# Kernel optimization log

Measured on AMD Instinct MI355X. Metric: run time of the kernel, lower is better.

## Reference

```python
import jax, jax.numpy as jnp
import numpy as np

B, L, D = 2, 2048, 2048        # batch, seqlen, d_model
DIN, N, R, K = 4096, 16, 128, 4  # d_inner, d_state, dt_rank, d_conv


def setup_inputs() -> dict:
    key = jax.random.key(0)
    ks = jax.random.split(key, 9)
    hidden_states = jax.random.normal(ks[0], (B, L, D), dtype=jnp.float32) * 0.02
    in_proj_w = jax.random.normal(ks[1], (2 * DIN, D), dtype=jnp.float32) * (1.0 / np.sqrt(D))
    conv1d_w = jax.random.normal(ks[2], (DIN, K), dtype=jnp.float32) * (1.0 / np.sqrt(DIN))
    x_proj_w = jax.random.normal(ks[3], (R + 2 * N, DIN), dtype=jnp.float32) * (1.0 / np.sqrt(DIN))
    dt_proj_w = jax.random.normal(ks[4], (DIN, R), dtype=jnp.float32) * (1.0 / np.sqrt(R))
    # dt_proj_bias init: inverse-softplus of dt ~ LogUniform(1e-3, 1e-1), as in init_dtprojbias
    dt = jnp.exp(jax.random.uniform(ks[5], (DIN,)) * (np.log(0.1) - np.log(0.001)) + np.log(0.001))
    dt = jnp.clip(dt, 1e-4, None)
    dt_proj_bias = dt + jnp.log(-jnp.expm1(-dt))
    # A_log init: log(arange(1..N)) broadcast over d_inner (init_A)
    A_log = jnp.broadcast_to(jnp.log(jnp.arange(1, N + 1, dtype=jnp.float32)), (DIN, N))
    D_param = jnp.ones((DIN,), dtype=jnp.float32)
    out_proj_w = jax.random.normal(ks[6], (D, DIN), dtype=jnp.float32) * (1.0 / np.sqrt(DIN))
    return {
        "hidden_states": hidden_states, "in_proj_w": in_proj_w, "conv1d_w": conv1d_w,
        "x_proj_w": x_proj_w, "dt_proj_w": dt_proj_w, "dt_proj_bias": dt_proj_bias,
        "A_log": A_log, "D_param": D_param, "out_proj_w": out_proj_w,
    }


def _mamba_forward(hidden_states, in_proj_w, conv1d_w, x_proj_w, dt_proj_w,
                   dt_proj_bias, A_log, D_param, out_proj_w):
    b, l, _ = hidden_states.shape
    # in_proj: (b,l,d_model) -> (b,l,2*d_inner), split into x and gate z
    xz = jnp.einsum("bld,ed->ble", hidden_states, in_proj_w)
    x, z = jnp.split(xz, 2, axis=-1)  # each (b,l,d_inner)

    # depthwise causal conv1d along l, no bias, then SiLU
    xp = jnp.pad(x, ((0, 0), (K - 1, 0), (0, 0)))
    xc = sum(conv1d_w[:, k] * xp[:, k:k + l, :] for k in range(K))  # (b,l,d_inner)
    xc = jax.nn.silu(xc)

    # x_proj -> dt_rank + 2*d_state, split into dt, B, C
    x_dbl = jnp.einsum("bld,ed->ble", xc, x_proj_w)
    dt_r = x_dbl[..., :R]                    # (b,l,R)
    Bc = x_dbl[..., R:R + N]                 # (b,l,N)
    Cc = x_dbl[..., R + N:]                  # (b,l,N)
    delta = jax.nn.softplus(jnp.einsum("blr,dr->bld", dt_r, dt_proj_w) + dt_proj_bias)  # (b,l,d_inner)

    A = -jnp.exp(A_log)  # (d_inner, N)

    # selective scan: h_t = exp(delta_t*A)*h_{t-1} + delta_t*x_t*B_t; y_t = <h_t, C_t>
    def step(h, inp):
        delta_t, B_t, C_t, x_t = inp  # (b,d), (b,n), (b,n), (b,d)
        dA = jnp.exp(delta_t[..., None] * A)                 # (b,d,n)
        h = h * dA + (delta_t * x_t)[..., None] * B_t[:, None, :]
        y_t = jnp.einsum("bdn,bn->bd", h, C_t)
        return h, y_t

    inputs = (jnp.swapaxes(delta, 0, 1), jnp.swapaxes(Bc, 0, 1),
              jnp.swapaxes(Cc, 0, 1), jnp.swapaxes(xc, 0, 1))
    h0 = jnp.zeros((b, DIN, N), dtype=xc.dtype)
    _, y = jax.lax.scan(step, h0, inputs)     # y: (l,b,d_inner)
    y = jnp.swapaxes(y, 0, 1)                 # (b,l,d_inner)

    y = y + xc * D_param                      # skip term
    y = y * jax.nn.silu(z)                    # gating
    return jnp.einsum("bld,ed->ble", y, out_proj_w)  # (b,l,d_model)


def reference(hidden_states, in_proj_w, conv1d_w, x_proj_w, dt_proj_w,
              dt_proj_bias, A_log, D_param, out_proj_w):
    return _mamba_forward(hidden_states, in_proj_w, conv1d_w, x_proj_w, dt_proj_w,
                          dt_proj_bias, A_log, D_param, out_proj_w)
```

## Files before the change

### kernel.cpp

```cpp
#include <hip/hip_runtime.h>
#include <math.h>

#define DIN   4096
#define NST   16
#define RR    128
#define LSEQ  2048
#define NTOK  4096
#define BB    2
#define CHUNK 64
#define NCH   (LSEQ / CHUNK)
#define KSPL  8
#define KC    (DIN / KSPL)

typedef __attribute__((ext_vector_type(8))) short short8;
typedef __attribute__((ext_vector_type(4))) float f32x4;

__device__ __forceinline__ float sigmoidf_(float x) { return 1.f / (1.f + __expf(-x)); }
__device__ __forceinline__ float softplusf_(float x) {
    return fmaxf(x, 0.f) + log1pf(__expf(-fabsf(x)));
}
__device__ __forceinline__ unsigned short f2bf_(float f) {
    unsigned u = __float_as_uint(f);
    return (unsigned short)((u + 0x7FFFu + ((u >> 16) & 1u)) >> 16);
}
__device__ __forceinline__ void gld_lds16_(const unsigned short* g, unsigned short* l) {
    __builtin_amdgcn_global_load_lds((const __attribute__((address_space(1))) unsigned int*)g,
                                     (__attribute__((address_space(3))) unsigned int*)l,
                                     16, 0, 0);
}

__global__ __launch_bounds__(256)
void f2bf_kernel(const float* __restrict__ src, unsigned short* __restrict__ dst, int n8)
{
    int i = blockIdx.x * 256 + threadIdx.x;
    if (i >= n8) return;
    const float4* s = (const float4*)src + 2 * (size_t)i;
    float4 a = s[0], b = s[1];
    union { unsigned short u[8]; uint4 v; } o;
    o.u[0] = f2bf_(a.x); o.u[1] = f2bf_(a.y); o.u[2] = f2bf_(a.z); o.u[3] = f2bf_(a.w);
    o.u[4] = f2bf_(b.x); o.u[5] = f2bf_(b.y); o.u[6] = f2bf_(b.z); o.u[7] = f2bf_(b.w);
    ((uint4*)dst)[i] = o.v;
}


#define BAR()        asm volatile("s_barrier" ::: "memory")
#define WAIT_LGKM0() asm volatile("s_waitcnt lgkmcnt(0)" ::: "memory")
#define WAIT_VM(n)   asm volatile("s_waitcnt vmcnt(" #n ")" ::: "memory")


#define RD_A(P, mh) do { _Pragma("unroll") \
  for (int ii = 0; ii < 4; ++ii) { \
      aF[ii][0] = *(const short8*)((P) + (mh)*8192 + ii*2048 + co0); \
      aF[ii][1] = *(const short8*)((P) + (mh)*8192 + ii*2048 + co1); } } while (0)

#define RD_B(P, nh, DST) do { _Pragma("unroll") \
  for (int jj = 0; jj < 2; ++jj) { \
      DST[jj][0] = *(const short8*)((P) + (nh)*4096 + jj*2048 + co0); \
      DST[jj][1] = *(const short8*)((P) + (nh)*4096 + jj*2048 + co1); } } while (0)

#define MFMA_Q(mh, nh, BF) do { __builtin_amdgcn_s_setprio(1); _Pragma("unroll") \
  for (int ii = 0; ii < 4; ++ii) { _Pragma("unroll") \
    for (int jj = 0; jj < 2; ++jj) { _Pragma("unroll") \
      for (int ks = 0; ks < 2; ++ks) \
        acc[(mh)*4+ii][(nh)*2+jj] = __builtin_amdgcn_mfma_f32_16x16x32_bf16( \
            aF[ii][ks], BF[jj][ks], acc[(mh)*4+ii][(nh)*2+jj], 0, 0, 0); } } \
  __builtin_amdgcn_s_setprio(0); } while (0)

#define STGLD(gbase, sbase, h, l, tile) \
  gld_lds16_(gbase + (size_t)((h)*128 + (l)*64) * K + (size_t)(tile)*64, \
             (unsigned short*)(sbase + (h)*16384 + (l)*8192))

#define ITER(t, PREF) do { \
   \
  RD_A(pA0, 0); RD_B(pB0c, 0, bA); \
  STGLD(gA0, sA1, 1, 0, (t)+1); STGLD(gA0, sA1, 1, 1, (t)+1); \
  BAR(); WAIT_LGKM0(); MFMA_Q(0, 0, bA); BAR(); \
   \
  RD_B(pB0c, 1, bB); \
  BAR(); WAIT_LGKM0(); MFMA_Q(0, 1, bB); BAR(); \
   \
  RD_A(pA0, 1); \
  if (PREF) { STGLD(gB0, sB0, 0, 0, (t)+2); STGLD(gB0, sB0, 0, 1, (t)+2); } \
  BAR(); WAIT_LGKM0(); MFMA_Q(1, 1, bB); BAR(); \
   \
  if (PREF) { STGLD(gA0, sA0, 0, 0, (t)+2); STGLD(gA0, sA0, 0, 1, (t)+2); \
              STGLD(gB0, sB0, 1, 0, (t)+2); STGLD(gB0, sB0, 1, 1, (t)+2); } \
  BAR(); WAIT_LGKM0(); MFMA_Q(1, 0, bA); \
  if (PREF) { WAIT_VM(6); } else { WAIT_VM(0); } \
  BAR(); \
   \
  RD_A(pA1, 0); RD_B(pB1c, 0, bA); \
  if (PREF) { STGLD(gA0, sA0, 1, 0, (t)+2); STGLD(gA0, sA0, 1, 1, (t)+2); } \
  BAR(); WAIT_LGKM0(); MFMA_Q(0, 0, bA); BAR(); \
   \
  RD_B(pB1c, 1, bB); \
  BAR(); WAIT_LGKM0(); MFMA_Q(0, 1, bB); BAR(); \
   \
  RD_A(pA1, 1); \
  if (PREF) { STGLD(gB0, sB1, 0, 0, (t)+3); STGLD(gB0, sB1, 0, 1, (t)+3); } \
  BAR(); WAIT_LGKM0(); MFMA_Q(1, 1, bB); BAR(); \
   \
  if (PREF) { STGLD(gA0, sA1, 0, 0, (t)+3); STGLD(gA0, sA1, 0, 1, (t)+3); \
              STGLD(gB0, sB1, 1, 0, (t)+3); STGLD(gB0, sB1, 1, 1, (t)+3); } \
  BAR(); WAIT_LGKM0(); MFMA_Q(1, 0, bA); \
  if (PREF) { WAIT_VM(6); } else { WAIT_VM(0); } \
  BAR(); \
} while (0)

template<int MODE>
__global__ __launch_bounds__(512)
void gemm256(const unsigned short* __restrict__ A, const unsigned short* __restrict__ W,
             float* __restrict__ C, int K, int ldc, float* __restrict__ C2,
             int nbx, int fx)
{
    __shared__ __align__(16) unsigned short sm[65536];
    char* smb = (char*)sm;

    const int tid = threadIdx.x;
    const int ln  = tid & 63;
    const int wv  = tid >> 6;
    const int wm  = wv >> 2;
    const int wn  = wv & 3;
    const int m15 = ln & 15;
    const int q   = ln >> 4;

    const int bid = blockIdx.x;
    const int xcd = bid & 7;
    const int idx = bid >> 3;
    const int cw  = nbx / fx;
    const int chh = (gridDim.x >> 3) / cw;
    const int bn_i = (xcd % fx) * cw  + idx % cw;
    const int bm_i = (xcd / fx) * chh + idx / cw;
    const int bm  = bm_i << 8;
    const int bn  = bn_i << 8;

    const int co0 = (q * 16) ^ ((m15 & 7) << 4);
    const int co1 = co0 ^ 64;
    const int ra_base = wm * 16384 + m15 * 128;
    const int rb_base = wn * 8192  + m15 * 128;
    const char* pA0  = smb + ra_base;
    const char* pA1  = smb + 65536 + ra_base;
    const char* pB0c = smb + 32768 + rb_base;
    const char* pB1c = smb + 98304 + rb_base;

    char* sA0 = smb +          tid * 16;
    char* sB0 = smb + 32768  + tid * 16;
    char* sA1 = smb + 65536  + tid * 16;
    char* sB1 = smb + 98304  + tid * 16;
    const int srow  = tid >> 3;
    const int secol = (((tid & 7) ^ ((tid >> 3) & 7)) * 8);
    const unsigned short* gA0 = A + (size_t)(bm + srow) * K + secol;
    const unsigned short* gB0 = W + (size_t)(bn + srow) * K + secol;

    f32x4  acc[8][4] = {};
    short8 aF[4][2], bA[2][2], bB[2][2];

    const int KT = K >> 6;

    STGLD(gA0, sA0, 0, 0, 0); STGLD(gA0, sA0, 0, 1, 0);
    STGLD(gA0, sA0, 1, 0, 0); STGLD(gA0, sA0, 1, 1, 0);
    STGLD(gB0, sB0, 0, 0, 0); STGLD(gB0, sB0, 0, 1, 0);
    STGLD(gB0, sB0, 1, 0, 0); STGLD(gB0, sB0, 1, 1, 0);
    STGLD(gA0, sA1, 0, 0, 1); STGLD(gA0, sA1, 0, 1, 1);
    STGLD(gB0, sB1, 0, 0, 1); STGLD(gB0, sB1, 0, 1, 1);
    STGLD(gB0, sB1, 1, 0, 1); STGLD(gB0, sB1, 1, 1, 1);
    WAIT_VM(6);
    BAR();

    for (int t = 0; t < KT - 2; t += 2) ITER(t, 1);
    ITER(KT - 2, 0);

    float* Cp = C;
    int bcol = bn;
    if (MODE == 2 && bcol >= DIN) { Cp = C2; bcol -= DIN; }
    #pragma unroll
    for (int i = 0; i < 8; ++i) {
        int row = bm + wm * 128 + i * 16 + q * 4;
        #pragma unroll
        for (int j = 0; j < 4; ++j) {
            int col = bcol + wn * 64 + j * 16 + m15;
            #pragma unroll
            for (int r = 0; r < 4; ++r)
                Cp[(size_t)(row + r) * ldc + col] = acc[i][j][r];
        }
    }
}

template<int MODE>
__global__ __launch_bounds__(256)
void gemm_mfma_bt(const unsigned short* __restrict__ A, const unsigned short* __restrict__ W,
                  float* __restrict__ C, int K, int ldc,
                  const float* __restrict__ bias, float* __restrict__ C2)
{
    __shared__ unsigned short As[128 * 32];
    __shared__ unsigned short Ws[128 * 32];
    const int tid = threadIdx.x;
    const int bm = blockIdx.y << 7;
    int bn = blockIdx.x << 7;

    const int c0 = tid, c1 = tid + 256;
    const unsigned short* ga0 = A + (size_t)(bm + (c0 >> 2)) * K + (c0 & 3) * 8;
    const unsigned short* ga1 = A + (size_t)(bm + (c1 >> 2)) * K + (c1 & 3) * 8;
    const unsigned short* gw0 = W + (size_t)(bn + (c0 >> 2)) * K + (c0 & 3) * 8;
    const unsigned short* gw1 = W + (size_t)(bn + (c1 >> 2)) * K + (c1 & 3) * 8;
    unsigned short* la0 = &As[c0 * 8];
    unsigned short* la1 = &As[c1 * 8];
    unsigned short* lw0 = &Ws[c0 * 8];
    unsigned short* lw1 = &Ws[c1 * 8];

    const int ln  = tid & 63;
    const int wv  = tid >> 6;
    const int wm  = (wv >> 1) << 6;
    const int wn  = (wv & 1) << 6;
    const int m15 = ln & 15;
    const int q   = ln >> 4;

    f32x4 acc[4][4] = {};

    for (int k0 = 0; k0 < K; k0 += 32) {
        __syncthreads();
        gld_lds16_(ga0, la0); gld_lds16_(ga1, la1);
        gld_lds16_(gw0, lw0); gld_lds16_(gw1, lw1);
        ga0 += 32; ga1 += 32; gw0 += 32; gw1 += 32;
        __syncthreads();
        short8 af[4], wf[4];
        #pragma unroll
        for (int i = 0; i < 4; ++i)
            af[i] = *(const short8*)&As[(wm + i * 16 + m15) * 32 + q * 8];
        #pragma unroll
        for (int j = 0; j < 4; ++j)
            wf[j] = *(const short8*)&Ws[(wn + j * 16 + m15) * 32 + q * 8];
        #pragma unroll
        for (int i = 0; i < 4; ++i)
            #pragma unroll
            for (int j = 0; j < 4; ++j)
                acc[i][j] = __builtin_amdgcn_mfma_f32_16x16x32_bf16(af[i], wf[j],
                                                                    acc[i][j], 0, 0, 0);
    }

    float* Cp = C;
    if (MODE == 2 && bn >= DIN) { Cp = C2; bn -= DIN; }

    #pragma unroll
    for (int i = 0; i < 4; ++i)
        #pragma unroll
        for (int j = 0; j < 4; ++j) {
            int col = bn + wn + j * 16 + m15;
            #pragma unroll
            for (int r = 0; r < 4; ++r) {
                int row = bm + wm + i * 16 + q * 4 + r;
                float v = acc[i][j][r];
                if (MODE == 1) v = softplusf_(v + bias[col]);
                Cp[(size_t)row * ldc + col] = v;
            }
        }
}

__global__ __launch_bounds__(256)
void gemm_kspl_kernel(const float* __restrict__ A, const float* __restrict__ W,
                      float* __restrict__ partial)
{
    __shared__ float As[16][66];
    __shared__ float Ws[16][162];
    const int tid = threadIdx.x;
    const int tx = tid & 15;
    const int ty = tid >> 4;
    const int bm = blockIdx.x << 6;
    const int k0 = blockIdx.y * KC;

    float acc[4][10] = {};

    for (int kt = 0; kt < KC; kt += 16) {
        float2 a2[2];
        #pragma unroll
        for (int i = 0; i < 2; ++i) {
            int idx = tid + 256 * i;
            int row = idx >> 3, kofs = (idx & 7) * 2;
            a2[i] = *(const float2*)&A[(size_t)(bm + row) * DIN + k0 + kt + kofs];
        }
        float2 w2[5];
        #pragma unroll
        for (int i = 0; i < 5; ++i) {
            int idx = tid + 256 * i;
            int wrow = idx >> 3, wk = (idx & 7) * 2;
            w2[i] = *(const float2*)&W[(size_t)wrow * DIN + k0 + kt + wk];
        }
        __syncthreads();
        #pragma unroll
        for (int i = 0; i < 2; ++i) {
            int idx = tid + 256 * i;
            int row = idx >> 3, kofs = (idx & 7) * 2;
            As[kofs][row] = a2[i].x; As[kofs + 1][row] = a2[i].y;
        }
        #pragma unroll
        for (int i = 0; i < 5; ++i) {
            int idx = tid + 256 * i;
            int wrow = idx >> 3, wk = (idx & 7) * 2;
            Ws[wk][wrow] = w2[i].x; Ws[wk + 1][wrow] = w2[i].y;
        }
        __syncthreads();
        #pragma unroll
        for (int kk = 0; kk < 16; ++kk) {
            float2 av0 = *(const float2*)&As[kk][ty * 4];
            float2 av1 = *(const float2*)&As[kk][ty * 4 + 2];
            float a[4] = {av0.x, av0.y, av1.x, av1.y};
            float w[10];
            #pragma unroll
            for (int j = 0; j < 5; ++j) {
                float2 wv = *(const float2*)&Ws[kk][tx * 10 + 2 * j];
                w[2 * j] = wv.x; w[2 * j + 1] = wv.y;
            }
            #pragma unroll
            for (int i = 0; i < 4; ++i)
                #pragma unroll
                for (int j = 0; j < 10; ++j)
                    acc[i][j] = fmaf(a[i], w[j], acc[i][j]);
        }
        __syncthreads();
    }

    float* po = partial + (size_t)blockIdx.y * NTOK * 160;
    #pragma unroll
    for (int i = 0; i < 4; ++i) {
        int r = bm + ty * 4 + i;
        #pragma unroll
        for (int j = 0; j < 5; ++j)
            *(float2*)&po[(size_t)r * 160 + tx * 10 + 2 * j] =
                make_float2(acc[i][2 * j], acc[i][2 * j + 1]);
    }
}

__global__ __launch_bounds__(256)
void kspl_reduce_kernel(const float* __restrict__ partial, float* __restrict__ xdbl,
                        unsigned short* __restrict__ dtr)
{
    int idx = blockIdx.x * 256 + threadIdx.x;
    float s = 0.f;
    #pragma unroll
    for (int k = 0; k < KSPL; ++k)
        s += partial[(size_t)k * NTOK * 160 + idx];
    xdbl[idx] = s;
    int row = idx / 160;
    int col = idx - row * 160;
    if (col < RR) dtr[(size_t)row * RR + col] = f2bf_(s);
}

__global__ __launch_bounds__(256)
void conv_silu_kernel(const float* __restrict__ x, const float* __restrict__ cw,
                      float* __restrict__ xc)
{
    int idx = blockIdx.x * 256 + threadIdx.x;
    int d = idx & (DIN - 1);
    int tok = idx >> 12;
    int t = tok & (LSEQ - 1);
    float w0 = cw[d * 4 + 0], w1 = cw[d * 4 + 1];
    float w2 = cw[d * 4 + 2], w3 = cw[d * 4 + 3];
    const float* xp = x + (size_t)tok * DIN + d;
    float acc = w3 * xp[0];
    if (t >= 1) acc = fmaf(w2, xp[-DIN], acc);
    if (t >= 2) acc = fmaf(w1, xp[-2 * DIN], acc);
    if (t >= 3) acc = fmaf(w0, xp[-3 * DIN], acc);
    xc[idx] = acc * sigmoidf_(acc);
}

__global__ __launch_bounds__(256)
void scan_part1_kernel(const float* __restrict__ delta, const float* __restrict__ xc,
                       const float* __restrict__ xdbl, const float* __restrict__ A_log,
                       float* __restrict__ hloc, float* __restrict__ ssum)
{
    int d = blockIdx.x * 256 + threadIdx.x;
    int c = blockIdx.y;
    int b = blockIdx.z;
    float A[NST], h[NST];
    #pragma unroll
    for (int n = 0; n < NST; ++n) {
        A[n] = -__expf(A_log[d * NST + n]);
        h[n] = 0.f;
    }
    float s = 0.f;
    int tok = b * LSEQ + c * CHUNK;
    for (int t = 0; t < CHUNK; ++t, ++tok) {
        float dv = delta[(size_t)tok * DIN + d];
        float xv = xc[(size_t)tok * DIN + d];
        const float* bc = xdbl + (size_t)tok * 160 + RR;
        float dx = dv * xv;
        s += dv;
        #pragma unroll
        for (int n = 0; n < NST; ++n)
            h[n] = fmaf(h[n], __expf(dv * A[n]), dx * bc[n]);
    }
    size_t base = (size_t)(b * NCH + c) * NST * DIN + d;
    #pragma unroll
    for (int n = 0; n < NST; ++n) hloc[base + (size_t)n * DIN] = h[n];
    ssum[(size_t)(b * NCH + c) * DIN + d] = s;
}

__global__ __launch_bounds__(256)
void scan_part2_kernel(float* __restrict__ hloc, const float* __restrict__ ssum,
                       const float* __restrict__ A_log)
{
    int idx = blockIdx.x * 256 + threadIdx.x;
    int b = idx >> 12;
    int d = idx & (DIN - 1);
    float A[NST], hin[NST];
    #pragma unroll
    for (int n = 0; n < NST; ++n) {
        A[n] = -__expf(A_log[d * NST + n]);
        hin[n] = 0.f;
    }
    for (int c = 0; c < NCH; ++c) {
        size_t base = (size_t)(b * NCH + c) * NST * DIN + d;
        float s = ssum[(size_t)(b * NCH + c) * DIN + d];
        #pragma unroll
        for (int n = 0; n < NST; ++n) {
            float hl = hloc[base + (size_t)n * DIN];
            hloc[base + (size_t)n * DIN] = hin[n];
            hin[n] = fmaf(hin[n], __expf(A[n] * s), hl);
        }
    }
}

__global__ __launch_bounds__(256)
void scan_part3_kernel(const float* __restrict__ delta, float* __restrict__ xcy,
                       const float* __restrict__ xdbl, const float* __restrict__ z,
                       const float* __restrict__ A_log, const float* __restrict__ Dp,
                       const float* __restrict__ hin_buf)
{
    int d = blockIdx.x * 256 + threadIdx.x;
    int c = blockIdx.y;
    int b = blockIdx.z;
    float A[NST], h[NST];
    size_t base = (size_t)(b * NCH + c) * NST * DIN + d;
    #pragma unroll
    for (int n = 0; n < NST; ++n) {
        A[n] = -__expf(A_log[d * NST + n]);
        h[n] = hin_buf[base + (size_t)n * DIN];
    }
    float Dv = Dp[d];
    int tok = b * LSEQ + c * CHUNK;
    for (int t = 0; t < CHUNK; ++t, ++tok) {
        float dv = delta[(size_t)tok * DIN + d];
        float xv = xcy[(size_t)tok * DIN + d];
        float zv = z[(size_t)tok * DIN + d];
        const float* bc = xdbl + (size_t)tok * 160 + RR;
        float dx = dv * xv;
        float y = 0.f;
        #pragma unroll
        for (int n = 0; n < NST; ++n) {
            h[n] = fmaf(h[n], __expf(dv * A[n]), dx * bc[n]);
            y = fmaf(h[n], bc[NST + n], y);
        }
        y = (y + xv * Dv) * (zv * sigmoidf_(zv));
        xcy[(size_t)tok * DIN + d] = y;
    }
}

extern "C" void kernel_launch(void* const* d_in, const int* in_sizes, int n_in,
                              void* d_out, int out_size, void* d_ws, size_t ws_size,
                              hipStream_t stream)
{
    const float* hidden     = (const float*)d_in[0];
    const float* in_proj_w  = (const float*)d_in[1];
    const float* conv_w     = (const float*)d_in[2];
    const float* x_proj_w   = (const float*)d_in[3];
    const float* dt_proj_w  = (const float*)d_in[4];
    const float* dt_bias    = (const float*)d_in[5];
    const float* A_log      = (const float*)d_in[6];
    const float* D_param    = (const float*)d_in[7];
    const float* out_proj_w = (const float*)d_in[8];
    float* out = (float*)d_out;

    const size_t BIG = (size_t)NTOK * DIN * sizeof(float);
    char* ws = (char*)d_ws;
    float* xbuf = (float*)(ws);
    float* xc   = (float*)(ws + BIG);
    float* zbuf = (float*)(ws + 2 * BIG);
    float* xdbl = (float*)(ws + 3 * BIG);
    float* delta = xbuf;

    unsigned short* w_in_bf  = (unsigned short*)xc;
    unsigned short* hid_bf   = (unsigned short*)out;
    unsigned short* y_bf     = (unsigned short*)xbuf;
    unsigned short* w_out_bf = (unsigned short*)zbuf;

    float* xpart = out;
    unsigned short* dtr_bf = (unsigned short*)(out + (size_t)KSPL * NTOK * 160);
    unsigned short* dtw_bf = dtr_bf + (size_t)NTOK * RR;
    float* hloc  = out;
    float* ssum  = out + (size_t)BB * NCH * NST * DIN;

    f2bf_kernel<<<8192, 256, 0, stream>>>(in_proj_w, w_in_bf, (2 * DIN * 2048) / 8);
    f2bf_kernel<<<4096, 256, 0, stream>>>(hidden, hid_bf, (NTOK * 2048) / 8);
    gemm256<2><<<512, 512, 0, stream>>>(hid_bf, w_in_bf, xbuf, 2048, DIN, zbuf, 32, 4);
    conv_silu_kernel<<<(NTOK * DIN) / 256, 256, 0, stream>>>(xbuf, conv_w, xc);
    gemm_kspl_kernel<<<dim3(NTOK / 64, KSPL), 256, 0, stream>>>(xc, x_proj_w, xpart);
    kspl_reduce_kernel<<<(NTOK * 160) / 256, 256, 0, stream>>>(xpart, xdbl, dtr_bf);
    f2bf_kernel<<<256, 256, 0, stream>>>(dt_proj_w, dtw_bf, (DIN * RR) / 8);
    gemm_mfma_bt<1><<<dim3(32, 32), 256, 0, stream>>>(dtr_bf, dtw_bf, delta,
                                                      RR, DIN, dt_bias, nullptr);
    scan_part1_kernel<<<dim3(DIN / 256, NCH, BB), 256, 0, stream>>>(delta, xc, xdbl,
                                                                    A_log, hloc, ssum);
    scan_part2_kernel<<<(BB * DIN) / 256, 256, 0, stream>>>(hloc, ssum, A_log);
    scan_part3_kernel<<<dim3(DIN / 256, NCH, BB), 256, 0, stream>>>(delta, xc, xdbl,
                                                                    zbuf, A_log, D_param, hloc);
    f2bf_kernel<<<8192, 256, 0, stream>>>(xc, y_bf, (NTOK * DIN) / 8);
    f2bf_kernel<<<4096, 256, 0, stream>>>(out_proj_w, w_out_bf, (2048 * DIN) / 8);
    gemm256<0><<<128, 512, 0, stream>>>(y_bf, w_out_bf, out, 4096, 2048, nullptr, 8, 2);
}
```

Baseline: 744.4 us.

## Split-K the out_proj GEMM and prefetch LDS fragments across MFMA phases

The out_proj GEMM previously launched only 128 blocks on a 256-CU-class GPU. It now splits K into two halves (MODE 3, 256 blocks), writes the second half's partial into a scratch buffer (xc), and sums the halves with a new float4 add kernel. Separately, the GEMM main loop is reordered so LDS fragment reads for the next quarter are issued right after the current MFMA group, with the first reads hoisted before the loop. This overlaps LDS latency with matrix math and removes some barrier stalls. The cost is an extra 32MB read-modify-write pass and more code in the barrier schedule.

```diff
diff --git a/kernel.cpp b/kernel.cpp
--- a/kernel.cpp
+++ b/kernel.cpp
@@ -42,6 +42,17 @@
     ((uint4*)dst)[i] = o.v;
 }
 
+__global__ __launch_bounds__(256)
+void add_f4_kernel(float* __restrict__ dst, const float* __restrict__ src, int n4)
+{
+    int i = blockIdx.x * 256 + threadIdx.x;
+    if (i >= n4) return;
+    float4 a = ((const float4*)dst)[i];
+    float4 b = ((const float4*)src)[i];
+    a.x += b.x; a.y += b.y; a.z += b.z; a.w += b.w;
+    ((float4*)dst)[i] = a;
+}
+
 
 #define BAR()        asm volatile("s_barrier" ::: "memory")
 #define WAIT_LGKM0() asm volatile("s_waitcnt lgkmcnt(0)" ::: "memory")
@@ -72,45 +83,51 @@
 
 #define ITER(t, PREF) do { \
    \
-  RD_A(pA0, 0); RD_B(pB0c, 0, bA); \
   STGLD(gA0, sA1, 1, 0, (t)+1); STGLD(gA0, sA1, 1, 1, (t)+1); \
-  BAR(); WAIT_LGKM0(); MFMA_Q(0, 0, bA); BAR(); \
-   \
-  RD_B(pB0c, 1, bB); \
-  BAR(); WAIT_LGKM0(); MFMA_Q(0, 1, bB); BAR(); \
-   \
-  RD_A(pA0, 1); \
+  BAR(); WAIT_LGKM0(); MFMA_Q(0, 0, bA); \
+  RD_B(pB0c, 1, bB);                     \
+  BAR(); \
+   \
+  BAR(); WAIT_LGKM0(); MFMA_Q(0, 1, bB); \
+  RD_A(pA0, 1);                          \
+  BAR(); \
+   \
   if (PREF) { STGLD(gB0, sB0, 0, 0, (t)+2); STGLD(gB0, sB0, 0, 1, (t)+2); } \
-  BAR(); WAIT_LGKM0(); MFMA_Q(1, 1, bB); BAR(); \
+  BAR(); WAIT_LGKM0(); MFMA_Q(1, 1, bB); \
+  BAR(); \
    \
   if (PREF) { STGLD(gA0, sA0, 0, 0, (t)+2); STGLD(gA0, sA0, 0, 1, (t)+2); \
               STGLD(gB0, sB0, 1, 0, (t)+2); STGLD(gB0, sB0, 1, 1, (t)+2); } \
   BAR(); WAIT_LGKM0(); MFMA_Q(1, 0, bA); \
   if (PREF) { WAIT_VM(6); } else { WAIT_VM(0); } \
-  BAR(); \
-   \
-  RD_A(pA1, 0); RD_B(pB1c, 0, bA); \
+  RD_A(pA1, 0); RD_B(pB1c, 0, bA);       \
+  BAR(); \
+   \
   if (PREF) { STGLD(gA0, sA0, 1, 0, (t)+2); STGLD(gA0, sA0, 1, 1, (t)+2); } \
-  BAR(); WAIT_LGKM0(); MFMA_Q(0, 0, bA); BAR(); \
-   \
-  RD_B(pB1c, 1, bB); \
-  BAR(); WAIT_LGKM0(); MFMA_Q(0, 1, bB); BAR(); \
-   \
-  RD_A(pA1, 1); \
+  BAR(); WAIT_LGKM0(); MFMA_Q(0, 0, bA); \
+  RD_B(pB1c, 1, bB);                     \
+  BAR(); \
+   \
+  BAR(); WAIT_LGKM0(); MFMA_Q(0, 1, bB); \
+  RD_A(pA1, 1);                          \
+  BAR(); \
+   \
   if (PREF) { STGLD(gB0, sB1, 0, 0, (t)+3); STGLD(gB0, sB1, 0, 1, (t)+3); } \
-  BAR(); WAIT_LGKM0(); MFMA_Q(1, 1, bB); BAR(); \
+  BAR(); WAIT_LGKM0(); MFMA_Q(1, 1, bB); \
+  BAR(); \
    \
   if (PREF) { STGLD(gA0, sA1, 0, 0, (t)+3); STGLD(gA0, sA1, 0, 1, (t)+3); \
               STGLD(gB0, sB1, 1, 0, (t)+3); STGLD(gB0, sB1, 1, 1, (t)+3); } \
   BAR(); WAIT_LGKM0(); MFMA_Q(1, 0, bA); \
   if (PREF) { WAIT_VM(6); } else { WAIT_VM(0); } \
+  if (PREF) { RD_A(pA0, 0); RD_B(pB0c, 0, bA); } \
   BAR(); \
 } while (0)
 
 template<int MODE>
 __global__ __launch_bounds__(512)
 void gemm256(const unsigned short* __restrict__ A, const unsigned short* __restrict__ W,
-             float* __restrict__ C, int K, int ldc, float* __restrict__ C2,
+             float* __restrict__ C, int K, int KL, int ldc, float* __restrict__ C2,
              int nbx, int fx)
 {
     __shared__ __align__(16) unsigned short sm[65536];
@@ -130,7 +147,9 @@
     const int cw  = nbx / fx;
     const int chh = (gridDim.x >> 3) / cw;
     const int bn_i = (xcd % fx) * cw  + idx % cw;
-    const int bm_i = (xcd / fx) * chh + idx / cw;
+    int bm_i = (xcd / fx) * chh + idx / cw;
+    int kh = 0;
+    if (MODE == 3) { kh = bm_i >> 4; bm_i &= 15; }
     const int bm  = bm_i << 8;
     const int bn  = bn_i << 8;
 
@@ -149,13 +168,13 @@
     char* sB1 = smb + 98304  + tid * 16;
     const int srow  = tid >> 3;
     const int secol = (((tid & 7) ^ ((tid >> 3) & 7)) * 8);
-    const unsigned short* gA0 = A + (size_t)(bm + srow) * K + secol;
-    const unsigned short* gB0 = W + (size_t)(bn + srow) * K + secol;
+    const unsigned short* gA0 = A + (size_t)(bm + srow) * K + secol + (size_t)kh * KL;
+    const unsigned short* gB0 = W + (size_t)(bn + srow) * K + secol + (size_t)kh * KL;
 
     f32x4  acc[8][4] = {};
     short8 aF[4][2], bA[2][2], bB[2][2];
 
-    const int KT = K >> 6;
+    const int KT = KL >> 6;
 
     STGLD(gA0, sA0, 0, 0, 0); STGLD(gA0, sA0, 0, 1, 0);
     STGLD(gA0, sA0, 1, 0, 0); STGLD(gA0, sA0, 1, 1, 0);
@@ -166,6 +185,7 @@
     STGLD(gB0, sB1, 1, 0, 1); STGLD(gB0, sB1, 1, 1, 1);
     WAIT_VM(6);
     BAR();
+    RD_A(pA0, 0); RD_B(pB0c, 0, bA);
 
     for (int t = 0; t < KT - 2; t += 2) ITER(t, 1);
     ITER(KT - 2, 0);
@@ -173,6 +193,7 @@
     float* Cp = C;
     int bcol = bn;
     if (MODE == 2 && bcol >= DIN) { Cp = C2; bcol -= DIN; }
+    if (MODE == 3 && kh) Cp = C2;
     #pragma unroll
     for (int i = 0; i < 8; ++i) {
         int row = bm + wm * 128 + i * 16 + q * 4;
@@ -491,7 +512,8 @@
 
     f2bf_kernel<<<8192, 256, 0, stream>>>(in_proj_w, w_in_bf, (2 * DIN * 2048) / 8);
     f2bf_kernel<<<4096, 256, 0, stream>>>(hidden, hid_bf, (NTOK * 2048) / 8);
-    gemm256<2><<<512, 512, 0, stream>>>(hid_bf, w_in_bf, xbuf, 2048, DIN, zbuf, 32, 4);
+    gemm256<2><<<512, 512, 0, stream>>>(hid_bf, w_in_bf, xbuf, 2048, 2048, DIN,
+                                        zbuf, 32, 4);
     conv_silu_kernel<<<(NTOK * DIN) / 256, 256, 0, stream>>>(xbuf, conv_w, xc);
     gemm_kspl_kernel<<<dim3(NTOK / 64, KSPL), 256, 0, stream>>>(xc, x_proj_w, xpart);
     kspl_reduce_kernel<<<(NTOK * 160) / 256, 256, 0, stream>>>(xpart, xdbl, dtr_bf);
@@ -505,5 +527,7 @@
                                                                     zbuf, A_log, D_param, hloc);
     f2bf_kernel<<<8192, 256, 0, stream>>>(xc, y_bf, (NTOK * DIN) / 8);
     f2bf_kernel<<<4096, 256, 0, stream>>>(out_proj_w, w_out_bf, (2048 * DIN) / 8);
-    gemm256<0><<<128, 512, 0, stream>>>(y_bf, w_out_bf, out, 4096, 2048, nullptr, 8, 2);
-}
+    gemm256<3><<<256, 512, 0, stream>>>(y_bf, w_out_bf, out, 4096, 2048, 2048,
+                                        xc, 8, 2);
+    add_f4_kernel<<<8192, 256, 0, stream>>>(out, xc, (NTOK * 2048) / 4);
+}
```

Result: no change. 740.7 us (-0.5%).
